# Performance work log

Measured on AMD Instinct MI355X. Metric: run time of the kernel, lower is better.

The kernel has to match this reference:

```python
import jax, jax.numpy as jnp
import numpy as np

# Config (matches init_kwargs)
B, DIM = 16, 768
HEADS, DHEAD = 12, 64
H_MEM, W_MEM = 16, 16           # memory grid; N = 256 tokens
MAX_AH, MAX_AW = 3, 3
N = H_MEM * W_MEM


def _area_pool(t):
    """t: [B', N, D] laid out on an H_MEM x W_MEM grid.
    Returns (area_sums [B', M, D], area_sizes [M]) over all rectangle sizes
    (ah, aw) with 1<=ah<=MAX_AH, 1<=aw<=MAX_AW, at every valid position,
    via a 2D integral image (summed-area table)."""
    Bp, _, D = t.shape
    g = t.reshape(Bp, H_MEM, W_MEM, D)
    I = jnp.cumsum(jnp.cumsum(g, axis=1), axis=2)
    I = jnp.pad(I, ((0, 0), (1, 0), (1, 0), (0, 0)))  # [B', H+1, W+1, D]
    sums, sizes = [], []
    for ah in range(1, MAX_AH + 1):
        for aw in range(1, MAX_AW + 1):
            s = (I[:, ah:, aw:] - I[:, :-ah, aw:]
                 - I[:, ah:, :-aw] + I[:, :-ah, :-aw])  # [B', H-ah+1, W-aw+1, D]
            n_pos = s.shape[1] * s.shape[2]
            sums.append(s.reshape(Bp, n_pos, D))
            sizes.append(np.full((n_pos,), float(ah * aw), dtype=np.float32))
    return jnp.concatenate(sums, axis=1), jnp.asarray(np.concatenate(sizes))


def setup_inputs() -> dict:
    key = jax.random.key(0)
    ks = jax.random.split(key, 10)
    s = 0.02
    d = dict(
        x=jax.random.normal(ks[0], (B, N, DIM), jnp.float32),
        # to_qkv: Linear(dim, 3*dim, bias=False); stored as (in, out)
        w_qkv=jax.random.normal(ks[1], (DIM, 3 * DIM), jnp.float32) * s,
        # per-head q/k/v projections (dim -> heads*dim_head) with bias
        w_q=jax.random.normal(ks[2], (DIM, HEADS * DHEAD), jnp.float32) * s,
        b_q=jnp.zeros((HEADS * DHEAD,), jnp.float32),
        w_k=jax.random.normal(ks[3], (DIM, HEADS * DHEAD), jnp.float32) * s,
        b_k=jnp.zeros((HEADS * DHEAD,), jnp.float32),
        w_v=jax.random.normal(ks[4], (DIM, HEADS * DHEAD), jnp.float32) * s,
        b_v=jnp.zeros((HEADS * DHEAD,), jnp.float32),
        # output projection (heads*dim_head -> dim)
        w_o=jax.random.normal(ks[5], (HEADS * DHEAD, DIM), jnp.float32) * s,
        b_o=jnp.zeros((DIM,), jnp.float32),
    )
    return d


def reference(x, w_qkv, w_q, b_q, w_k, b_k, w_v, b_v, w_o, b_o):
    # QKV projection + split: 'b n (qkv d) -> qkv b n d'
    qkv = x @ w_qkv                               # [B, N, 3*DIM]
    q, k, v = jnp.split(qkv, 3, axis=-1)          # each [B, N, DIM]

    def to_heads(t, w, b):                        # 'b n (h d) -> (b h) n d'
        return ((t @ w + b)
                .reshape(B, N, HEADS, DHEAD)
                .transpose(0, 2, 1, 3)
                .reshape(B * HEADS, N, DHEAD))

    qh = to_heads(q, w_q, b_q)
    kh = to_heads(k, w_k, b_k)
    vh = to_heads(v, w_v, b_v)

    # Area keys: mean over each area; area values: sum over each area.
    k_sum, sizes = _area_pool(kh)                 # [BH, M, d], [M]
    k_area = k_sum / sizes[None, :, None]
    v_area, _ = _area_pool(vh)                    # [BH, M, d]

    logits = jnp.einsum('bqd,bmd->bqm', qh, k_area)   # [BH, N, M]
    weights = jax.nn.softmax(logits, axis=-1)
    out = jnp.einsum('bqm,bmd->bqd', weights, v_area)  # [BH, N, d]

    # '(b h) n d -> b n (h d)' then output projection
    out = (out.reshape(B, HEADS, N, DHEAD)
              .transpose(0, 2, 1, 3)
              .reshape(B, N, HEADS * DHEAD))
    return out @ w_o + b_o
```

## Files before the change

### kernel.cpp

```cpp
#include <hip/hip_runtime.h>
#include <hip/hip_bf16.h>

typedef __hip_bfloat16 bf16;
typedef __attribute__((ext_vector_type(8))) short short8b;
typedef __attribute__((ext_vector_type(4))) short short4b;
typedef __attribute__((ext_vector_type(4))) float f32x4;

#define NAREA 2025
#define NAREA_PAD 2048

static __device__ __forceinline__ float b2f(bf16 x) { return __bfloat162float(x); }
static __device__ __forceinline__ short f2bs(float f) {
  bf16 h = __float2bfloat16(f);
  return *(short*)&h;
}

__global__ __launch_bounds__(256) void k_cast(
    const float* __restrict__ x, const float* __restrict__ wqkv,
    bf16* __restrict__ xb, bf16* __restrict__ wqkvb)
{
  int idx = (blockIdx.x * 256 + threadIdx.x) * 4;
  const int NX = 4096 * 768;
  float4 v;
  bf16* d;
  if (idx < NX) { v = *(const float4*)(x + idx); d = xb + idx; }
  else { v = *(const float4*)(wqkv + (idx - NX)); d = wqkvb + (idx - NX); }
  short4b s = {f2bs(v.x), f2bs(v.y), f2bs(v.z), f2bs(v.w)};
  *(short4b*)d = s;
}

__global__ __launch_bounds__(256) void k_tcast(
    const float* __restrict__ s0, const float* __restrict__ s1,
    const float* __restrict__ s2, bf16* __restrict__ d0,
    bf16* __restrict__ d1, bf16* __restrict__ d2)
{
  __shared__ float tile[32][33];
  int z = blockIdx.z;
  const float* src = (z == 0) ? s0 : (z == 1) ? s1 : s2;
  bf16* dst = (z == 0) ? d0 : (z == 1) ? d1 : d2;
  int r0 = blockIdx.y * 32, c0 = blockIdx.x * 32;
  int lx = threadIdx.x & 31, ly = threadIdx.x >> 5;
#pragma unroll
  for (int yy = 0; yy < 4; ++yy)
    tile[ly + yy * 8][lx] = src[(size_t)(r0 + ly + yy * 8) * 768 + c0 + lx];
  __syncthreads();
#pragma unroll
  for (int yy = 0; yy < 4; ++yy)
    dst[(size_t)(c0 + ly + yy * 8) * 768 + r0 + lx] =
        __float2bfloat16(tile[lx][ly + yy * 8]);
}


__global__ __launch_bounds__(256) void k_combine_m(
    const bf16* __restrict__ wqkvb, const bf16* __restrict__ wqT,
    const bf16* __restrict__ wkT, const bf16* __restrict__ wvT,
    bf16* __restrict__ WcTb)
{
  __shared__ __align__(16) short As[2][128 * 32];
  __shared__ __align__(16) short Bs[2][128 * 32];
  const int t3 = blockIdx.z;
  const bf16* BT = (t3 == 0) ? wqT : (t3 == 1) ? wkT : wvT;
  const int m0 = blockIdx.y * 128, n0 = blockIdx.x * 128;
  const int tid = threadIdx.x, lane = tid & 63, w = tid >> 6;
  const int tt = lane & 15, q4 = lane >> 4;
  const int moff = (w & 1) * 64, noff = (w >> 1) * 64;
  const int r_a = tid >> 2, kc = (tid & 3) * 8;

  f32x4 acc[4][4];
#pragma unroll
  for (int i = 0; i < 4; ++i)
#pragma unroll
    for (int j = 0; j < 4; ++j) acc[i][j] = (f32x4){0.f, 0.f, 0.f, 0.f};

  uint4 ra0 = *(const uint4*)(wqkvb + (size_t)(m0 + r_a) * 2304 + t3 * 768 + kc);
  uint4 ra1 = *(const uint4*)(wqkvb + (size_t)(m0 + r_a + 64) * 2304 + t3 * 768 + kc);
  uint4 rb0 = *(const uint4*)(BT + (size_t)(n0 + r_a) * 768 + kc);
  uint4 rb1 = *(const uint4*)(BT + (size_t)(n0 + r_a + 64) * 768 + kc);

  for (int it = 0; it < 24; ++it) {
    short* as = As[it & 1];
    short* bs = Bs[it & 1];
    *(uint4*)&as[r_a * 32 + kc] = ra0;
    *(uint4*)&as[(r_a + 64) * 32 + kc] = ra1;
    *(uint4*)&bs[r_a * 32 + kc] = rb0;
    *(uint4*)&bs[(r_a + 64) * 32 + kc] = rb1;
    if (it < 23) {
      int k0 = (it + 1) * 32;
      ra0 = *(const uint4*)(wqkvb + (size_t)(m0 + r_a) * 2304 + t3 * 768 + k0 + kc);
      ra1 = *(const uint4*)(wqkvb + (size_t)(m0 + r_a + 64) * 2304 + t3 * 768 + k0 + kc);
      rb0 = *(const uint4*)(BT + (size_t)(n0 + r_a) * 768 + k0 + kc);
      rb1 = *(const uint4*)(BT + (size_t)(n0 + r_a + 64) * 768 + k0 + kc);
    }
    __syncthreads();
    short8b afr[4], bfr[4];
#pragma unroll
    for (int mt = 0; mt < 4; ++mt)
      afr[mt] = *(const short8b*)&as[(moff + mt * 16 + tt) * 32 + q4 * 8];
#pragma unroll
    for (int nt = 0; nt < 4; ++nt)
      bfr[nt] = *(const short8b*)&bs[(noff + nt * 16 + tt) * 32 + q4 * 8];
#pragma unroll
    for (int mt = 0; mt < 4; ++mt)
#pragma unroll
      for (int nt = 0; nt < 4; ++nt)
        acc[mt][nt] = __builtin_amdgcn_mfma_f32_16x16x32_bf16(afr[mt], bfr[nt], acc[mt][nt], 0, 0, 0);
  }

  bf16* C = WcTb + (size_t)t3 * 768 * 768;
#pragma unroll
  for (int nt = 0; nt < 4; ++nt) {
    int n = n0 + noff + nt * 16 + tt;
#pragma unroll
    for (int mt = 0; mt < 4; ++mt) {
      int mb = m0 + moff + mt * 16 + q4 * 4;
      short4b v = {f2bs(acc[mt][nt][0]), f2bs(acc[mt][nt][1]),
                   f2bs(acc[mt][nt][2]), f2bs(acc[mt][nt][3])};
      *(short4b*)&C[(size_t)n * 768 + mb] = v;
    }
  }
}

__global__ __launch_bounds__(256) void k_proj_m(
    const bf16* __restrict__ xb, const bf16* __restrict__ WcTb,
    const float* __restrict__ bq, const float* __restrict__ bk,
    const float* __restrict__ bv,
    bf16* __restrict__ qh, bf16* __restrict__ kh, bf16* __restrict__ vh)
{
  __shared__ __align__(16) short As[2][128 * 32];
  __shared__ __align__(16) short Bs[2][128 * 32];
  const int t3 = blockIdx.z;
  const bf16* BT = WcTb + (size_t)t3 * 768 * 768;
  const float* bias = (t3 == 0) ? bq : (t3 == 1) ? bk : bv;
  bf16* dst = (t3 == 0) ? qh : (t3 == 1) ? kh : vh;
  const int m0 = blockIdx.y * 128, n0 = blockIdx.x * 128;
  const int tid = threadIdx.x, lane = tid & 63, w = tid >> 6;
  const int tt = lane & 15, q4 = lane >> 4;
  const int moff = (w & 1) * 64, noff = (w >> 1) * 64;
  const int r_a = tid >> 2, kc = (tid & 3) * 8;

  f32x4 acc[4][4];
#pragma unroll
  for (int i = 0; i < 4; ++i)
#pragma unroll
    for (int j = 0; j < 4; ++j) acc[i][j] = (f32x4){0.f, 0.f, 0.f, 0.f};

  uint4 ra0 = *(const uint4*)(xb + (size_t)(m0 + r_a) * 768 + kc);
  uint4 ra1 = *(const uint4*)(xb + (size_t)(m0 + r_a + 64) * 768 + kc);
  uint4 rb0 = *(const uint4*)(BT + (size_t)(n0 + r_a) * 768 + kc);
  uint4 rb1 = *(const uint4*)(BT + (size_t)(n0 + r_a + 64) * 768 + kc);

  for (int it = 0; it < 24; ++it) {
    short* as = As[it & 1];
    short* bs = Bs[it & 1];
    *(uint4*)&as[r_a * 32 + kc] = ra0;
    *(uint4*)&as[(r_a + 64) * 32 + kc] = ra1;
    *(uint4*)&bs[r_a * 32 + kc] = rb0;
    *(uint4*)&bs[(r_a + 64) * 32 + kc] = rb1;
    if (it < 23) {
      int k0 = (it + 1) * 32;
      ra0 = *(const uint4*)(xb + (size_t)(m0 + r_a) * 768 + k0 + kc);
      ra1 = *(const uint4*)(xb + (size_t)(m0 + r_a + 64) * 768 + k0 + kc);
      rb0 = *(const uint4*)(BT + (size_t)(n0 + r_a) * 768 + k0 + kc);
      rb1 = *(const uint4*)(BT + (size_t)(n0 + r_a + 64) * 768 + k0 + kc);
    }
    __syncthreads();
    short8b afr[4], bfr[4];
#pragma unroll
    for (int mt = 0; mt < 4; ++mt)
      afr[mt] = *(const short8b*)&as[(moff + mt * 16 + tt) * 32 + q4 * 8];
#pragma unroll
    for (int nt = 0; nt < 4; ++nt)
      bfr[nt] = *(const short8b*)&bs[(noff + nt * 16 + tt) * 32 + q4 * 8];
#pragma unroll
    for (int mt = 0; mt < 4; ++mt)
#pragma unroll
      for (int nt = 0; nt < 4; ++nt)
        acc[mt][nt] = __builtin_amdgcn_mfma_f32_16x16x32_bf16(afr[mt], bfr[nt], acc[mt][nt], 0, 0, 0);
  }

#pragma unroll
  for (int nt = 0; nt < 4; ++nt) {
    int c = n0 + noff + nt * 16 + tt;
    float bv = bias[c];
    int h = c >> 6, d = c & 63;
#pragma unroll
    for (int mt = 0; mt < 4; ++mt) {
#pragma unroll
      for (int r = 0; r < 4; ++r) {
        int m = m0 + moff + mt * 16 + q4 * 4 + r;
        dst[(((size_t)((m >> 8) * 12 + h)) << 14) + ((m & 255) << 6) + d] =
            __float2bfloat16(acc[mt][nt][r] + bv);
      }
    }
  }
}

__global__ __launch_bounds__(256) void k_out_m(
    const bf16* __restrict__ attno, const bf16* __restrict__ woT,
    const float* __restrict__ bo, float* __restrict__ out)
{
  __shared__ __align__(16) short As[2][128 * 32];
  __shared__ __align__(16) short Bs[2][128 * 32];
  const int m0 = blockIdx.y * 128, n0 = blockIdx.x * 128;
  const int tid = threadIdx.x, lane = tid & 63, w = tid >> 6;
  const int tt = lane & 15, q4 = lane >> 4;
  const int moff = (w & 1) * 64, noff = (w >> 1) * 64;
  const int r_a = tid >> 2, kc = (tid & 3) * 8;

  f32x4 acc[4][4];
#pragma unroll
  for (int i = 0; i < 4; ++i)
#pragma unroll
    for (int j = 0; j < 4; ++j) acc[i][j] = (f32x4){0.f, 0.f, 0.f, 0.f};

  int m_a0 = m0 + r_a, m_a1 = m0 + r_a + 64;
  uint4 ra0 = *(const uint4*)(attno + (((size_t)((m_a0 >> 8) * 12 + (kc >> 6))) << 14) + ((m_a0 & 255) << 6) + (kc & 63));
  uint4 ra1 = *(const uint4*)(attno + (((size_t)((m_a1 >> 8) * 12 + (kc >> 6))) << 14) + ((m_a1 & 255) << 6) + (kc & 63));
  uint4 rb0 = *(const uint4*)(woT + (size_t)(n0 + r_a) * 768 + kc);
  uint4 rb1 = *(const uint4*)(woT + (size_t)(n0 + r_a + 64) * 768 + kc);

  for (int it = 0; it < 24; ++it) {
    short* as = As[it & 1];
    short* bs = Bs[it & 1];
    *(uint4*)&as[r_a * 32 + kc] = ra0;
    *(uint4*)&as[(r_a + 64) * 32 + kc] = ra1;
    *(uint4*)&bs[r_a * 32 + kc] = rb0;
    *(uint4*)&bs[(r_a + 64) * 32 + kc] = rb1;
    if (it < 23) {
      int k = (it + 1) * 32 + kc;
      ra0 = *(const uint4*)(attno + (((size_t)((m_a0 >> 8) * 12 + (k >> 6))) << 14) + ((m_a0 & 255) << 6) + (k & 63));
      ra1 = *(const uint4*)(attno + (((size_t)((m_a1 >> 8) * 12 + (k >> 6))) << 14) + ((m_a1 & 255) << 6) + (k & 63));
      rb0 = *(const uint4*)(woT + (size_t)(n0 + r_a) * 768 + k);
      rb1 = *(const uint4*)(woT + (size_t)(n0 + r_a + 64) * 768 + k);
    }
    __syncthreads();
    short8b afr[4], bfr[4];
#pragma unroll
    for (int mt = 0; mt < 4; ++mt)
      afr[mt] = *(const short8b*)&as[(moff + mt * 16 + tt) * 32 + q4 * 8];
#pragma unroll
    for (int nt = 0; nt < 4; ++nt)
      bfr[nt] = *(const short8b*)&bs[(noff + nt * 16 + tt) * 32 + q4 * 8];
#pragma unroll
    for (int mt = 0; mt < 4; ++mt)
#pragma unroll
      for (int nt = 0; nt < 4; ++nt)
        acc[mt][nt] = __builtin_amdgcn_mfma_f32_16x16x32_bf16(afr[mt], bfr[nt], acc[mt][nt], 0, 0, 0);
  }

#pragma unroll
  for (int nt = 0; nt < 4; ++nt) {
    int c = n0 + noff + nt * 16 + tt;
    float bv = bo[c];
#pragma unroll
    for (int mt = 0; mt < 4; ++mt)
#pragma unroll
      for (int r = 0; r < 4; ++r) {
        int m = m0 + moff + mt * 16 + q4 * 4 + r;
        out[(size_t)m * 768 + c] = acc[mt][nt][r] + bv;
      }
  }
}

__global__ __launch_bounds__(256) void k_rect(int4* __restrict__ rectG,
                                              float* __restrict__ invG)
{
  int m = blockIdx.x * 256 + threadIdx.x;
  if (m >= NAREA_PAD) return;
  int4 rc = make_int4(0, 0, 0, 0);
  float iv = 0.f;
  if (m < NAREA) {
    int rem = m, ah = 1, aw = 1, found = 0;
    for (int a = 1; a <= 3 && !found; ++a)
      for (int w = 1; w <= 3 && !found; ++w) {
        int np = (17 - a) * (17 - w);
        if (rem < np) { ah = a; aw = w; found = 1; }
        else rem -= np;
      }
    int cw = 17 - aw;
    int y = rem / cw, x = rem - y * cw;
    rc.x = (y * 17 + x) * 64;
    rc.y = (y * 17 + (x + aw)) * 64;
    rc.z = ((y + ah) * 17 + x) * 64;
    rc.w = ((y + ah) * 17 + (x + aw)) * 64;
    iv = 1.0f / (float)(ah * aw);
  }
  rectG[m] = rc;
  invG[m] = iv;
}

__global__ __launch_bounds__(128) void k_integral(
    const bf16* __restrict__ kh, const bf16* __restrict__ vh,
    float* __restrict__ Ik, float* __restrict__ Iv)
{
  int bh = blockIdx.x;
  int d = threadIdx.x & 63;
  bool isv = threadIdx.x >= 64;
  const bf16* src = (isv ? vh : kh) + ((size_t)bh << 14);
  float* dst = (isv ? Iv : Ik) + (size_t)bh * 18496;
  float prev[17];
#pragma unroll
  for (int i = 0; i < 17; ++i) prev[i] = 0.f;
#pragma unroll
  for (int xx = 0; xx < 17; ++xx) dst[xx * 64 + d] = 0.f;
#pragma unroll 1
  for (int y = 1; y <= 16; ++y) {
    dst[(y * 17) * 64 + d] = 0.f;
    float rs = 0.f;
#pragma unroll
    for (int xx = 1; xx <= 16; ++xx) {
      rs += b2f(src[((y - 1) * 16 + (xx - 1)) * 64 + d]);
      float cur = prev[xx] + rs;
      dst[(y * 17 + xx) * 64 + d] = cur;
      prev[xx] = cur;
    }
  }
}

__global__ __launch_bounds__(1024) void k_attn_m(
    const bf16* __restrict__ qh, const float* __restrict__ Ik,
    const float* __restrict__ Iv, const int4* __restrict__ rectG,
    const float* __restrict__ invG, bf16* __restrict__ attno)
{
  __shared__ __align__(16) short aK2[2][64 * 72];
  __shared__ __align__(16) short aVt2[2][64 * 72];
  __shared__ __align__(16) short Pb[16][16 * 72];

  const int tid = threadIdx.x;
  const int lane = tid & 63;
  const int w = tid >> 6;
  const int t = lane & 15;
  const int q4 = lane >> 4;
  const int bh = blockIdx.x;

  const float* Ikb = Ik + (size_t)bh * 18496;
  const float* Ivb = Iv + (size_t)bh * 18496;
  const bf16* qbase = qh + ((size_t)bh << 14);

  short8b qf0 = *(const short8b*)(qbase + (w * 16 + t) * 64 + q4 * 8);
  short8b qf1 = *(const short8b*)(qbase + (w * 16 + t) * 64 + 32 + q4 * 8);

  f32x4 O[4];
#pragma unroll
  for (int i = 0; i < 4; ++i) O[i] = (f32x4){0.f, 0.f, 0.f, 0.f};
  float l = 0.f;

  {
    short* aK = aK2[0];
    short* aVt = aVt2[0];
#pragma unroll
    for (int i = 0; i < 4; ++i) {
      int j = w * 4 + i;
      int4 rc = rectG[j];
      float iv = invG[j];
      float kc = Ikb[rc.w + lane] - Ikb[rc.y + lane] - Ikb[rc.z + lane] + Ikb[rc.x + lane];
      float vc = Ivb[rc.w + lane] - Ivb[rc.y + lane] - Ivb[rc.z + lane] + Ivb[rc.x + lane];
      aK[j * 72 + lane] = f2bs(kc * iv);
      aVt[lane * 72 + j] = f2bs(vc);
    }
  }

  for (int it = 0; it < 32; ++it) {
    __syncthreads();
    const short* aK = aK2[it & 1];
    const short* aVt = aVt2[it & 1];
    if (it + 1 < 32) {
      int t0n = (it + 1) * 64;
      short* aKn = aK2[(it + 1) & 1];
      short* aVtn = aVt2[(it + 1) & 1];
#pragma unroll
      for (int i = 0; i < 4; ++i) {
        int j = w * 4 + i;
        int4 rc = rectG[t0n + j];
        float iv = invG[t0n + j];
        float kc = Ikb[rc.w + lane] - Ikb[rc.y + lane] - Ikb[rc.z + lane] + Ikb[rc.x + lane];
        float vc = Ivb[rc.w + lane] - Ivb[rc.y + lane] - Ivb[rc.z + lane] + Ivb[rc.x + lane];
        aKn[j * 72 + lane] = f2bs(kc * iv);
        aVtn[lane * 72 + j] = f2bs(vc);
      }
    }

    const int t0 = it * 64;
    const bool edge = (t0 + 64 > NAREA);
#pragma unroll
    for (int at = 0; at < 4; ++at) {
      short8b af0 = *(const short8b*)&aK[(at * 16 + t) * 72 + q4 * 8];
      short8b af1 = *(const short8b*)&aK[(at * 16 + t) * 72 + 32 + q4 * 8];
      f32x4 s = (f32x4){0.f, 0.f, 0.f, 0.f};
      s = __builtin_amdgcn_mfma_f32_16x16x32_bf16(af0, qf0, s, 0, 0, 0);
      s = __builtin_amdgcn_mfma_f32_16x16x32_bf16(af1, qf1, s, 0, 0, 0);
      float p[4];
#pragma unroll
      for (int r = 0; r < 4; ++r) {
        p[r] = __expf(s[r]);
        if (edge && (t0 + at * 16 + q4 * 4 + r >= NAREA)) p[r] = 0.f;
      }
      l += (p[0] + p[1]) + (p[2] + p[3]);
      short4b pk = (short4b){f2bs(p[0]), f2bs(p[1]), f2bs(p[2]), f2bs(p[3])};
      *(short4b*)&Pb[w][t * 72 + at * 16 + q4 * 4] = pk;
    }
    short8b pf0 = *(const short8b*)&Pb[w][t * 72 + q4 * 8];
    short8b pf1 = *(const short8b*)&Pb[w][t * 72 + 32 + q4 * 8];
#pragma unroll
    for (int nt = 0; nt < 4; ++nt) {
      short8b vf0 = *(const short8b*)&aVt[(nt * 16 + t) * 72 + q4 * 8];
      short8b vf1 = *(const short8b*)&aVt[(nt * 16 + t) * 72 + 32 + q4 * 8];
      O[nt] = __builtin_amdgcn_mfma_f32_16x16x32_bf16(pf0, vf0, O[nt], 0, 0, 0);
      O[nt] = __builtin_amdgcn_mfma_f32_16x16x32_bf16(pf1, vf1, O[nt], 0, 0, 0);
    }
  }

  l += __shfl_xor(l, 16, 64);
  l += __shfl_xor(l, 32, 64);

  bf16* ob = attno + ((size_t)bh << 14);
#pragma unroll
  for (int r = 0; r < 4; ++r) {
    int qrow = q4 * 4 + r;
    float invl = 1.0f / __shfl(l, qrow, 64);
#pragma unroll
    for (int nt = 0; nt < 4; ++nt)
      ob[(w * 16 + qrow) * 64 + nt * 16 + t] = __float2bfloat16(O[nt][r] * invl);
  }
}

extern "C" void kernel_launch(void* const* d_in, const int* in_sizes, int n_in,
                              void* d_out, int out_size, void* d_ws, size_t ws_size,
                              hipStream_t stream) {
  const float* x    = (const float*)d_in[0];
  const float* wqkv = (const float*)d_in[1];
  const float* wq   = (const float*)d_in[2];
  const float* bq   = (const float*)d_in[3];
  const float* wk   = (const float*)d_in[4];
  const float* bk   = (const float*)d_in[5];
  const float* wv   = (const float*)d_in[6];
  const float* bv   = (const float*)d_in[7];
  const float* wo   = (const float*)d_in[8];
  const float* bo   = (const float*)d_in[9];
  float* out = (float*)d_out;

  char* ws = (char*)d_ws;
  char* ob = (char*)d_out;
  const size_t WC_B = 7077888;
  const size_t QH_B = 6291456;

  bf16* xb    = (bf16*)ob;
  bf16* WcTb  = (bf16*)(ob + QH_B);
  bf16* attno = (bf16*)ws;
  int4*  rectG = (int4*)(ws + QH_B);
  float* invG  = (float*)(ws + QH_B + 32768);
  bf16* qh = (bf16*)(ws + WC_B);
  bf16* kh = (bf16*)(ws + WC_B + QH_B);
  bf16* vh = (bf16*)(ws + WC_B + 2 * QH_B);
  bf16* wqkvb = (bf16*)(ws + WC_B);
  bf16* wqT   = (bf16*)(ws + WC_B + 3538944);
  bf16* wkT   = (bf16*)(ws + WC_B + 4718592);
  bf16* wvT   = (bf16*)(ws + WC_B + 5898240);
  float* Ik = (float*)(ws + WC_B + 3 * QH_B);
  float* Iv = Ik + 3551232;
  bf16* woT = (bf16*)(ws + WC_B + 3 * QH_B);

  k_cast<<<dim3(4800), 256, 0, stream>>>(x, wqkv, xb, wqkvb);
  k_tcast<<<dim3(24, 24, 3), 256, 0, stream>>>(wq, wk, wv, wqT, wkT, wvT);
  k_combine_m<<<dim3(6, 6, 3), 256, 0, stream>>>(wqkvb, wqT, wkT, wvT, WcTb);
  k_proj_m<<<dim3(6, 32, 3), 256, 0, stream>>>(xb, WcTb, bq, bk, bv, qh, kh, vh);
  k_rect<<<dim3(8), 256, 0, stream>>>(rectG, invG);
  k_integral<<<dim3(192), 128, 0, stream>>>(kh, vh, Ik, Iv);
  k_attn_m<<<dim3(192), 1024, 0, stream>>>(qh, Ik, Iv, rectG, invG, attno);
  k_tcast<<<dim3(24, 24, 1), 256, 0, stream>>>(wo, wo, wo, woT, woT, woT);
  k_out_m<<<dim3(6, 32), 256, 0, stream>>>(attno, woT, bo, out);
}
```

Measured before the change: 256.0 us.

## Merge prep kernels, parallelize integral image, prefetch area gathers into registers

Merges the cast, weight-transpose and rect-table kernels into one launch to cut launch count. Rewrites the integral-image kernel to use 1024 threads per (bh, k/v) block, with separate row and column scans in shared memory, replacing the old serial 64-thread scan. In the attention kernel, the global gathers for the next area tile are issued before the barrier into registers, and the transposed V writes are packed into 4-wide stores. The new integral kernel adds a large shared-memory footprint and barriers, and register prefetching raises register pressure in a 1024-thread kernel.

New measurement: 242.7 us. -5.2%, faster.

```diff
diff --git a/kernel.cpp b/kernel.cpp
--- a/kernel.cpp
+++ b/kernel.cpp
@@ -15,29 +15,73 @@
   return *(short*)&h;
 }
 
-__global__ __launch_bounds__(256) void k_cast(
+__global__ __launch_bounds__(256) void k_prep(
     const float* __restrict__ x, const float* __restrict__ wqkv,
-    bf16* __restrict__ xb, bf16* __restrict__ wqkvb)
-{
-  int idx = (blockIdx.x * 256 + threadIdx.x) * 4;
-  const int NX = 4096 * 768;
-  float4 v;
-  bf16* d;
-  if (idx < NX) { v = *(const float4*)(x + idx); d = xb + idx; }
-  else { v = *(const float4*)(wqkv + (idx - NX)); d = wqkvb + (idx - NX); }
-  short4b s = {f2bs(v.x), f2bs(v.y), f2bs(v.z), f2bs(v.w)};
-  *(short4b*)d = s;
-}
-
-__global__ __launch_bounds__(256) void k_tcast(
-    const float* __restrict__ s0, const float* __restrict__ s1,
-    const float* __restrict__ s2, bf16* __restrict__ d0,
-    bf16* __restrict__ d1, bf16* __restrict__ d2)
+    const float* __restrict__ wq, const float* __restrict__ wk,
+    const float* __restrict__ wv,
+    bf16* __restrict__ xb, bf16* __restrict__ wqkvb,
+    bf16* __restrict__ wqT, bf16* __restrict__ wkT, bf16* __restrict__ wvT,
+    int4* __restrict__ rectG, float* __restrict__ invG)
 {
   __shared__ float tile[32][33];
-  int z = blockIdx.z;
-  const float* src = (z == 0) ? s0 : (z == 1) ? s1 : s2;
-  bf16* dst = (z == 0) ? d0 : (z == 1) ? d1 : d2;
+  int b = blockIdx.x;
+  if (b < 4800) {
+    int idx = (b * 256 + threadIdx.x) * 4;
+    const int NX = 4096 * 768;
+    float4 v;
+    bf16* d;
+    if (idx < NX) { v = *(const float4*)(x + idx); d = xb + idx; }
+    else { v = *(const float4*)(wqkv + (idx - NX)); d = wqkvb + (idx - NX); }
+    short4b s = {f2bs(v.x), f2bs(v.y), f2bs(v.z), f2bs(v.w)};
+    *(short4b*)d = s;
+    return;
+  }
+  if (b < 6528) {
+    int r = b - 4800;
+    int z = r / 576; r -= z * 576;
+    int by = r / 24, bx = r - by * 24;
+    const float* src = (z == 0) ? wq : (z == 1) ? wk : wv;
+    bf16* dst = (z == 0) ? wqT : (z == 1) ? wkT : wvT;
+    int r0 = by * 32, c0 = bx * 32;
+    int lx = threadIdx.x & 31, ly = threadIdx.x >> 5;
+#pragma unroll
+    for (int yy = 0; yy < 4; ++yy)
+      tile[ly + yy * 8][lx] = src[(size_t)(r0 + ly + yy * 8) * 768 + c0 + lx];
+    __syncthreads();
+#pragma unroll
+    for (int yy = 0; yy < 4; ++yy)
+      dst[(size_t)(c0 + ly + yy * 8) * 768 + r0 + lx] =
+          __float2bfloat16(tile[lx][ly + yy * 8]);
+    return;
+  }
+  int m = (b - 6528) * 256 + threadIdx.x;
+  if (m >= NAREA_PAD) return;
+  int4 rc = make_int4(0, 0, 0, 0);
+  float iv = 0.f;
+  if (m < NAREA) {
+    int rem = m, ah = 1, aw = 1, found = 0;
+    for (int a = 1; a <= 3 && !found; ++a)
+      for (int w = 1; w <= 3 && !found; ++w) {
+        int np = (17 - a) * (17 - w);
+        if (rem < np) { ah = a; aw = w; found = 1; }
+        else rem -= np;
+      }
+    int cw = 17 - aw;
+    int y = rem / cw, xx = rem - y * cw;
+    rc.x = (y * 17 + xx) * 64;
+    rc.y = (y * 17 + (xx + aw)) * 64;
+    rc.z = ((y + ah) * 17 + xx) * 64;
+    rc.w = ((y + ah) * 17 + (xx + aw)) * 64;
+    iv = 1.0f / (float)(ah * aw);
+  }
+  rectG[m] = rc;
+  invG[m] = iv;
+}
+
+__global__ __launch_bounds__(256) void k_tcast1(
+    const float* __restrict__ src, bf16* __restrict__ dst)
+{
+  __shared__ float tile[32][33];
   int r0 = blockIdx.y * 32, c0 = blockIdx.x * 32;
   int lx = threadIdx.x & 31, ly = threadIdx.x >> 5;
 #pragma unroll
@@ -181,7 +225,7 @@
 #pragma unroll
   for (int nt = 0; nt < 4; ++nt) {
     int c = n0 + noff + nt * 16 + tt;
-    float bv = bias[c];
+    float bvv = bias[c];
     int h = c >> 6, d = c & 63;
 #pragma unroll
     for (int mt = 0; mt < 4; ++mt) {
@@ -189,7 +233,7 @@
       for (int r = 0; r < 4; ++r) {
         int m = m0 + moff + mt * 16 + q4 * 4 + r;
         dst[(((size_t)((m >> 8) * 12 + h)) << 14) + ((m & 255) << 6) + d] =
-            __float2bfloat16(acc[mt][nt][r] + bv);
+            __float2bfloat16(acc[mt][nt][r] + bvv);
       }
     }
   }
@@ -251,70 +295,54 @@
 #pragma unroll
   for (int nt = 0; nt < 4; ++nt) {
     int c = n0 + noff + nt * 16 + tt;
-    float bv = bo[c];
+    float bvv = bo[c];
 #pragma unroll
     for (int mt = 0; mt < 4; ++mt)
 #pragma unroll
       for (int r = 0; r < 4; ++r) {
         int m = m0 + moff + mt * 16 + q4 * 4 + r;
-        out[(size_t)m * 768 + c] = acc[mt][nt][r] + bv;
+        out[(size_t)m * 768 + c] = acc[mt][nt][r] + bvv;
       }
   }
 }
 
-__global__ __launch_bounds__(256) void k_rect(int4* __restrict__ rectG,
-                                              float* __restrict__ invG)
-{
-  int m = blockIdx.x * 256 + threadIdx.x;
-  if (m >= NAREA_PAD) return;
-  int4 rc = make_int4(0, 0, 0, 0);
-  float iv = 0.f;
-  if (m < NAREA) {
-    int rem = m, ah = 1, aw = 1, found = 0;
-    for (int a = 1; a <= 3 && !found; ++a)
-      for (int w = 1; w <= 3 && !found; ++w) {
-        int np = (17 - a) * (17 - w);
-        if (rem < np) { ah = a; aw = w; found = 1; }
-        else rem -= np;
-      }
-    int cw = 17 - aw;
-    int y = rem / cw, x = rem - y * cw;
-    rc.x = (y * 17 + x) * 64;
-    rc.y = (y * 17 + (x + aw)) * 64;
-    rc.z = ((y + ah) * 17 + x) * 64;
-    rc.w = ((y + ah) * 17 + (x + aw)) * 64;
-    iv = 1.0f / (float)(ah * aw);
-  }
-  rectG[m] = rc;
-  invG[m] = iv;
-}
-
-__global__ __launch_bounds__(128) void k_integral(
+__global__ __launch_bounds__(1024) void k_integral_p(
     const bf16* __restrict__ kh, const bf16* __restrict__ vh,
     float* __restrict__ Ik, float* __restrict__ Iv)
 {
-  int bh = blockIdx.x;
-  int d = threadIdx.x & 63;
-  bool isv = threadIdx.x >= 64;
+  __shared__ float sat[17 * 17 * 64];
+  int bh = blockIdx.x >> 1;
+  bool isv = blockIdx.x & 1;
   const bf16* src = (isv ? vh : kh) + ((size_t)bh << 14);
   float* dst = (isv ? Iv : Ik) + (size_t)bh * 18496;
-  float prev[17];
-#pragma unroll
-  for (int i = 0; i < 17; ++i) prev[i] = 0.f;
-#pragma unroll
-  for (int xx = 0; xx < 17; ++xx) dst[xx * 64 + d] = 0.f;
-#pragma unroll 1
-  for (int y = 1; y <= 16; ++y) {
-    dst[(y * 17) * 64 + d] = 0.f;
-    float rs = 0.f;
-#pragma unroll
-    for (int xx = 1; xx <= 16; ++xx) {
-      rs += b2f(src[((y - 1) * 16 + (xx - 1)) * 64 + d]);
-      float cur = prev[xx] + rs;
-      dst[(y * 17 + xx) * 64 + d] = cur;
-      prev[xx] = cur;
-    }
-  }
+  int tid = threadIdx.x;
+  int d = tid & 63;
+  int row = tid >> 6;
+  {
+    float run = 0.f;
+    sat[((row + 1) * 17) * 64 + d] = 0.f;
+#pragma unroll
+    for (int xx = 0; xx < 16; ++xx) {
+      run += b2f(src[(row * 16 + xx) * 64 + d]);
+      sat[((row + 1) * 17 + (xx + 1)) * 64 + d] = run;
+    }
+    if (row == 0) {
+#pragma unroll
+      for (int xx = 0; xx < 17; ++xx) sat[xx * 64 + d] = 0.f;
+    }
+  }
+  __syncthreads();
+  {
+    int x = row + 1;
+    float run = 0.f;
+#pragma unroll
+    for (int y = 1; y <= 16; ++y) {
+      run += sat[(y * 17 + x) * 64 + d];
+      sat[(y * 17 + x) * 64 + d] = run;
+    }
+  }
+  __syncthreads();
+  for (int i = tid; i < 18496; i += 1024) dst[i] = sat[i];
 }
 
 __global__ __launch_bounds__(1024) void k_attn_m(
@@ -348,6 +376,7 @@
   {
     short* aK = aK2[0];
     short* aVt = aVt2[0];
+    short vp[4];
 #pragma unroll
     for (int i = 0; i < 4; ++i) {
       int j = w * 4 + i;
@@ -356,28 +385,37 @@
       float kc = Ikb[rc.w + lane] - Ikb[rc.y + lane] - Ikb[rc.z + lane] + Ikb[rc.x + lane];
       float vc = Ivb[rc.w + lane] - Ivb[rc.y + lane] - Ivb[rc.z + lane] + Ivb[rc.x + lane];
       aK[j * 72 + lane] = f2bs(kc * iv);
-      aVt[lane * 72 + j] = f2bs(vc);
-    }
-  }
-
+      vp[i] = f2bs(vc);
+    }
+    *(short4b*)&aVt[lane * 72 + w * 4] = (short4b){vp[0], vp[1], vp[2], vp[3]};
+  }
+
+  float kcr[4], vcr[4], ivr[4];
   for (int it = 0; it < 32; ++it) {
+    if (it + 1 < 32) {
+      int t0n = (it + 1) * 64;
+#pragma unroll
+      for (int i = 0; i < 4; ++i) {
+        int j = t0n + w * 4 + i;
+        int4 rc = rectG[j];
+        ivr[i] = invG[j];
+        kcr[i] = Ikb[rc.w + lane] - Ikb[rc.y + lane] - Ikb[rc.z + lane] + Ikb[rc.x + lane];
+        vcr[i] = Ivb[rc.w + lane] - Ivb[rc.y + lane] - Ivb[rc.z + lane] + Ivb[rc.x + lane];
+      }
+    }
     __syncthreads();
     const short* aK = aK2[it & 1];
     const short* aVt = aVt2[it & 1];
     if (it + 1 < 32) {
-      int t0n = (it + 1) * 64;
       short* aKn = aK2[(it + 1) & 1];
       short* aVtn = aVt2[(it + 1) & 1];
+      short vp[4];
 #pragma unroll
       for (int i = 0; i < 4; ++i) {
-        int j = w * 4 + i;
-        int4 rc = rectG[t0n + j];
-        float iv = invG[t0n + j];
-        float kc = Ikb[rc.w + lane] - Ikb[rc.y + lane] - Ikb[rc.z + lane] + Ikb[rc.x + lane];
-        float vc = Ivb[rc.w + lane] - Ivb[rc.y + lane] - Ivb[rc.z + lane] + Ivb[rc.x + lane];
-        aKn[j * 72 + lane] = f2bs(kc * iv);
-        aVtn[lane * 72 + j] = f2bs(vc);
+        aKn[(w * 4 + i) * 72 + lane] = f2bs(kcr[i] * ivr[i]);
+        vp[i] = f2bs(vcr[i]);
       }
+      *(short4b*)&aVtn[lane * 72 + w * 4] = (short4b){vp[0], vp[1], vp[2], vp[3]};
     }
 
     const int t0 = it * 64;
@@ -460,13 +498,12 @@
   float* Iv = Ik + 3551232;
   bf16* woT = (bf16*)(ws + WC_B + 3 * QH_B);
 
-  k_cast<<<dim3(4800), 256, 0, stream>>>(x, wqkv, xb, wqkvb);
-  k_tcast<<<dim3(24, 24, 3), 256, 0, stream>>>(wq, wk, wv, wqT, wkT, wvT);
+  k_prep<<<dim3(6536), 256, 0, stream>>>(x, wqkv, wq, wk, wv, xb, wqkvb,
+                                         wqT, wkT, wvT, rectG, invG);
   k_combine_m<<<dim3(6, 6, 3), 256, 0, stream>>>(wqkvb, wqT, wkT, wvT, WcTb);
   k_proj_m<<<dim3(6, 32, 3), 256, 0, stream>>>(xb, WcTb, bq, bk, bv, qh, kh, vh);
-  k_rect<<<dim3(8), 256, 0, stream>>>(rectG, invG);
-  k_integral<<<dim3(192), 128, 0, stream>>>(kh, vh, Ik, Iv);
+  k_integral_p<<<dim3(384), 1024, 0, stream>>>(kh, vh, Ik, Iv);
   k_attn_m<<<dim3(192), 1024, 0, stream>>>(qh, Ik, Iv, rectG, invG, attno);
-  k_tcast<<<dim3(24, 24, 1), 256, 0, stream>>>(wo, wo, wo, woT, woT, woT);
+  k_tcast1<<<dim3(24, 24), 256, 0, stream>>>(wo, woT);
   k_out_m<<<dim3(6, 32), 256, 0, stream>>>(attno, woT, bo, out);
 }
```
